# Performance work log

Measured on AMD Instinct MI355X. Metric: run time of the kernel, lower is better.

The kernel has to match this reference:

```python
import jax, jax.numpy as jnp
import numpy as np

DIM, WIDTH, POOL, BATCH, SEQ = 4096, 4, 512, 256, 16

def setup_inputs() -> dict:
    key = jax.random.key(0)
    k1, k2, k3, k4 = jax.random.split(key, 4)
    x = jax.random.normal(k1, (BATCH, SEQ, DIM), dtype=jnp.float32)
    conv_state = jax.random.normal(k2, (POOL, WIDTH - 1, DIM), dtype=jnp.float32)
    weight = jax.random.normal(k3, (WIDTH, DIM), dtype=jnp.float32)
    bias = jax.random.normal(k4, (DIM,), dtype=jnp.float32)
    conv_state_indices = jnp.arange(BATCH, dtype=jnp.int32)
    return {"x": x, "conv_state": conv_state, "weight": weight,
            "bias": bias, "conv_state_indices": conv_state_indices}

def reference(x, conv_state, weight, bias, conv_state_indices):
    # x: [b, s, d]; conv_state: [pool, width-1, d]; weight: [width, d]
    b, s, d = x.shape
    width = weight.shape[0]
    state = conv_state[conv_state_indices]            # gather: [b, width-1, d]
    x_new = jnp.concatenate([state, x], axis=1)       # [b, width-1+s, d]
    # depthwise causal conv, width taps (small fixed loop over taps)
    out = bias
    for k in range(width):
        out = out + x_new[:, k:k + s, :] * weight[k]  # [b, s, d]
    out = jax.nn.silu(out)                            # activation=True
    new_state = x_new[:, -(width - 1):, :]            # [b, width-1, d]
    updated_conv_state = conv_state.at[conv_state_indices].set(new_state)
    return out, updated_conv_state
```

## Files before the change

kernel.cpp:

```cpp
#include <hip/hip_runtime.h>

constexpr int DIM   = 4096;
constexpr int WIDTH = 4;
constexpr int POOL  = 512;
constexpr int BATCH = 256;
constexpr int SEQ   = 16;

constexpr int S_PER       = 8;
constexpr int D4_CHUNKS   = DIM / (4 * 256);
constexpr int BLK_PER_B   = D4_CHUNKS * 2;
constexpr int CONV_BLOCKS = BLK_PER_B * BATCH;

typedef float f32x4 __attribute__((ext_vector_type(4)));

__device__ __forceinline__ f32x4 ld4(const float* p) {
    return *reinterpret_cast<const f32x4*>(p);
}
__device__ __forceinline__ void st4(float* p, f32x4 v) {
    *reinterpret_cast<f32x4*>(p) = v;
}
__device__ __forceinline__ float fast_silu(float v) {
    return v * __builtin_amdgcn_rcpf(1.0f + __expf(-v));
}

__global__ __launch_bounds__(256, 4) void fused_conv_update_kernel(
    const float* __restrict__ x,
    const float* __restrict__ conv_state,
    const float* __restrict__ weight,
    const float* __restrict__ bias,
    const int*   __restrict__ idxs,
    float*       __restrict__ out,
    float*       __restrict__ out_state)
{
    const int blk   = blockIdx.x;
    const int b     = blk >> 3;
    const int rem   = blk & 7;
    const int chunk = rem >> 1;
    const int half  = rem & 1;
    const int d     = (chunk * 256 + threadIdx.x) * 4;
    const int idx   = idxs[b];

    const float* xb = x + (size_t)b * SEQ * DIM + d;

    f32x4 xv[S_PER + WIDTH - 1];
    if (half == 0) {
        const float* st = conv_state + (size_t)idx * (WIDTH - 1) * DIM + d;
        xv[0] = ld4(st + 0 * DIM);
        xv[1] = ld4(st + 1 * DIM);
        xv[2] = ld4(st + 2 * DIM);
#pragma unroll
        for (int t = 0; t < S_PER; ++t)
            xv[WIDTH - 1 + t] = ld4(xb + (size_t)t * DIM);
    } else {
#pragma unroll
        for (int t = 0; t < S_PER + WIDTH - 1; ++t)
            xv[t] = ld4(xb + (size_t)(S_PER - (WIDTH - 1) + t) * DIM);
    }

    const f32x4 w0 = ld4(weight + 0 * DIM + d);
    const f32x4 w1 = ld4(weight + 1 * DIM + d);
    const f32x4 w2 = ld4(weight + 2 * DIM + d);
    const f32x4 w3 = ld4(weight + 3 * DIM + d);
    const f32x4 bs = ld4(bias + d);

    const int row = blk >> 2;
    const int q   = blk & 3;
    constexpr int Q_FLOATS = (WIDTH - 1) * DIM / 4;
    const float* csrc = conv_state + (size_t)row * (WIDTH - 1) * DIM
                      + (size_t)q * Q_FLOATS + threadIdx.x * 4;
    f32x4 c0 = ld4(csrc + 0 * 1024);
    f32x4 c1 = ld4(csrc + 1 * 1024);
    f32x4 c2 = ld4(csrc + 2 * 1024);

    const int4 iv = *reinterpret_cast<const int4*>(idxs + (threadIdx.x & 63) * 4);
    const bool hit = (iv.x == row) | (iv.y == row) | (iv.z == row) | (iv.w == row);
    const bool skip = (__ballot(hit) != 0ull);

    __builtin_amdgcn_sched_barrier(0);

    float* ob = out + (size_t)b * SEQ * DIM + (size_t)half * S_PER * DIM + d;
#pragma unroll
    for (int s = 0; s < S_PER; ++s) {
        f32x4 acc = bs + xv[s] * w0 + xv[s + 1] * w1 + xv[s + 2] * w2 + xv[s + 3] * w3;
        acc.x = fast_silu(acc.x);
        acc.y = fast_silu(acc.y);
        acc.z = fast_silu(acc.z);
        acc.w = fast_silu(acc.w);
        st4(ob + (size_t)s * DIM, acc);
    }

    if (half == 1) {
        float* sd = out_state + (size_t)idx * (WIDTH - 1) * DIM + d;
        st4(sd + 0 * DIM, xv[S_PER + 0]);
        st4(sd + 1 * DIM, xv[S_PER + 1]);
        st4(sd + 2 * DIM, xv[S_PER + 2]);
    }

    if (!skip) {
        float* cdst = out_state + (size_t)row * (WIDTH - 1) * DIM
                    + (size_t)q * Q_FLOATS + threadIdx.x * 4;
        st4(cdst + 0 * 1024, c0);
        st4(cdst + 1 * 1024, c1);
        st4(cdst + 2 * 1024, c2);
    }
}

extern "C" void kernel_launch(void* const* d_in, const int* in_sizes, int n_in,
                              void* d_out, int out_size, void* d_ws, size_t ws_size,
                              hipStream_t stream)
{
    const float* x          = (const float*)d_in[0];
    const float* conv_state = (const float*)d_in[1];
    const float* weight     = (const float*)d_in[2];
    const float* bias       = (const float*)d_in[3];
    const int*   idxs       = (const int*)  d_in[4];

    float* out       = (float*)d_out;
    float* out_state = out + (size_t)BATCH * SEQ * DIM;

    fused_conv_update_kernel<<<CONV_BLOCKS, 256, 0, stream>>>(
        x, conv_state, weight, bias, idxs, out, out_state);
}
```

Baseline: 36.26 us.

## Process full sequence per thread with 2-wide vectors and skip unused state loads

Each thread now handles two channels across all 16 timesteps instead of four channels across half the sequence, removing the 3-row halo re-read of x in the second half-block. Block count stays the same, and launch bounds are raised to 8 blocks per SM. The pool-row copy loads are now issued only when the row is not overwritten, which saves reads for touched rows but makes those loads depend on the ballot result. The sched_barrier is removed. Loads and stores become 8-byte rather than 16-byte, which may lower per-instruction memory efficiency.

```diff
diff --git a/kernel.cpp b/kernel.cpp
--- a/kernel.cpp
+++ b/kernel.cpp
@@ -6,13 +6,18 @@
 constexpr int BATCH = 256;
 constexpr int SEQ   = 16;
 
-constexpr int S_PER       = 8;
-constexpr int D4_CHUNKS   = DIM / (4 * 256);
-constexpr int BLK_PER_B   = D4_CHUNKS * 2;
+constexpr int BLK_PER_B   = (DIM / 2) / 256;
 constexpr int CONV_BLOCKS = BLK_PER_B * BATCH;
 
+typedef float f32x2 __attribute__((ext_vector_type(2)));
 typedef float f32x4 __attribute__((ext_vector_type(4)));
 
+__device__ __forceinline__ f32x2 ld2(const float* p) {
+    return *reinterpret_cast<const f32x2*>(p);
+}
+__device__ __forceinline__ void st2(float* p, f32x2 v) {
+    *reinterpret_cast<f32x2*>(p) = v;
+}
 __device__ __forceinline__ f32x4 ld4(const float* p) {
     return *reinterpret_cast<const f32x4*>(p);
 }
@@ -23,7 +28,7 @@
     return v * __builtin_amdgcn_rcpf(1.0f + __expf(-v));
 }
 
-__global__ __launch_bounds__(256, 4) void fused_conv_update_kernel(
+__global__ __launch_bounds__(256, 8) void fused_conv_update_kernel(
     const float* __restrict__ x,
     const float* __restrict__ conv_state,
     const float* __restrict__ weight,
@@ -32,69 +37,58 @@
     float*       __restrict__ out,
     float*       __restrict__ out_state)
 {
-    const int blk   = blockIdx.x;
-    const int b     = blk >> 3;
-    const int rem   = blk & 7;
-    const int chunk = rem >> 1;
-    const int half  = rem & 1;
-    const int d     = (chunk * 256 + threadIdx.x) * 4;
-    const int idx   = idxs[b];
+    const int blk  = blockIdx.x;
+    const int b    = blk >> 3;
+    const int part = blk & (BLK_PER_B - 1);
+    const int d    = (part * 256 + threadIdx.x) * 2;
+    const int idx  = idxs[b];
 
     const float* xb = x + (size_t)b * SEQ * DIM + d;
+    const float* st = conv_state + (size_t)idx * (WIDTH - 1) * DIM + d;
 
-    f32x4 xv[S_PER + WIDTH - 1];
-    if (half == 0) {
-        const float* st = conv_state + (size_t)idx * (WIDTH - 1) * DIM + d;
-        xv[0] = ld4(st + 0 * DIM);
-        xv[1] = ld4(st + 1 * DIM);
-        xv[2] = ld4(st + 2 * DIM);
+    f32x2 xv[SEQ + WIDTH - 1];
+    xv[0] = ld2(st + 0 * DIM);
+    xv[1] = ld2(st + 1 * DIM);
+    xv[2] = ld2(st + 2 * DIM);
 #pragma unroll
-        for (int t = 0; t < S_PER; ++t)
-            xv[WIDTH - 1 + t] = ld4(xb + (size_t)t * DIM);
-    } else {
-#pragma unroll
-        for (int t = 0; t < S_PER + WIDTH - 1; ++t)
-            xv[t] = ld4(xb + (size_t)(S_PER - (WIDTH - 1) + t) * DIM);
-    }
+    for (int s = 0; s < SEQ; ++s)
+        xv[WIDTH - 1 + s] = ld2(xb + (size_t)s * DIM);
 
-    const f32x4 w0 = ld4(weight + 0 * DIM + d);
-    const f32x4 w1 = ld4(weight + 1 * DIM + d);
-    const f32x4 w2 = ld4(weight + 2 * DIM + d);
-    const f32x4 w3 = ld4(weight + 3 * DIM + d);
-    const f32x4 bs = ld4(bias + d);
+    const f32x2 w0 = ld2(weight + 0 * DIM + d);
+    const f32x2 w1 = ld2(weight + 1 * DIM + d);
+    const f32x2 w2 = ld2(weight + 2 * DIM + d);
+    const f32x2 w3 = ld2(weight + 3 * DIM + d);
+    const f32x2 bs = ld2(bias + d);
 
     const int row = blk >> 2;
     const int q   = blk & 3;
-    constexpr int Q_FLOATS = (WIDTH - 1) * DIM / 4;
-    const float* csrc = conv_state + (size_t)row * (WIDTH - 1) * DIM
-                      + (size_t)q * Q_FLOATS + threadIdx.x * 4;
-    f32x4 c0 = ld4(csrc + 0 * 1024);
-    f32x4 c1 = ld4(csrc + 1 * 1024);
-    f32x4 c2 = ld4(csrc + 2 * 1024);
-
     const int4 iv = *reinterpret_cast<const int4*>(idxs + (threadIdx.x & 63) * 4);
     const bool hit = (iv.x == row) | (iv.y == row) | (iv.z == row) | (iv.w == row);
     const bool skip = (__ballot(hit) != 0ull);
 
-    __builtin_amdgcn_sched_barrier(0);
+    constexpr int Q_FLOATS = (WIDTH - 1) * DIM / 4;
+    const float* csrc = conv_state + (size_t)row * (WIDTH - 1) * DIM
+                      + (size_t)q * Q_FLOATS + threadIdx.x * 4;
+    f32x4 c0, c1, c2;
+    if (!skip) {
+        c0 = ld4(csrc + 0 * 1024);
+        c1 = ld4(csrc + 1 * 1024);
+        c2 = ld4(csrc + 2 * 1024);
+    }
 
-    float* ob = out + (size_t)b * SEQ * DIM + (size_t)half * S_PER * DIM + d;
+    float* ob = out + (size_t)b * SEQ * DIM + d;
 #pragma unroll
-    for (int s = 0; s < S_PER; ++s) {
-        f32x4 acc = bs + xv[s] * w0 + xv[s + 1] * w1 + xv[s + 2] * w2 + xv[s + 3] * w3;
+    for (int s = 0; s < SEQ; ++s) {
+        f32x2 acc = bs + xv[s] * w0 + xv[s + 1] * w1 + xv[s + 2] * w2 + xv[s + 3] * w3;
         acc.x = fast_silu(acc.x);
         acc.y = fast_silu(acc.y);
-        acc.z = fast_silu(acc.z);
-        acc.w = fast_silu(acc.w);
-        st4(ob + (size_t)s * DIM, acc);
+        st2(ob + (size_t)s * DIM, acc);
     }
 
-    if (half == 1) {
-        float* sd = out_state + (size_t)idx * (WIDTH - 1) * DIM + d;
-        st4(sd + 0 * DIM, xv[S_PER + 0]);
-        st4(sd + 1 * DIM, xv[S_PER + 1]);
-        st4(sd + 2 * DIM, xv[S_PER + 2]);
-    }
+    float* sd = out_state + (size_t)idx * (WIDTH - 1) * DIM + d;
+    st2(sd + 0 * DIM, xv[SEQ + 0]);
+    st2(sd + 1 * DIM, xv[SEQ + 1]);
+    st2(sd + 2 * DIM, xv[SEQ + 2]);
 
     if (!skip) {
         float* cdst = out_state + (size_t)row * (WIDTH - 1) * DIM
```

After: 36.26 us. Within noise of the previous version (+0.0%).
